# Kernel optimization log

Measured on AMD Instinct MI355X. Metric: run time of the kernel, lower is better.

Reference implementation:

```python
import jax, jax.numpy as jnp
import numpy as np

EPS = 1e-7

def _sample_project(feat, pid, w1, b1, w2, b2):
    # feat: [B, C, H, W]; pid: [P] flat spatial indices into H*W
    B, C, H, W = feat.shape
    fr = jnp.transpose(feat, (0, 2, 3, 1)).reshape(B, H * W, C)  # [B, HW, C]
    x = fr[:, pid, :].reshape(B * pid.shape[0], C)               # gather -> [B*P, C]
    x = jnp.maximum(x @ w1 + b1, 0.0) @ w2 + b2                  # 2-layer MLP
    norm = jnp.sqrt(jnp.sum(x * x, axis=1, keepdims=True))       # L2 over channels
    return x / (norm + EPS)


def setup_inputs() -> dict:
    key = jax.random.key(0)
    ks = jax.random.split(key, 16)
    NC = 256
    shapes = [(16, 256, 128, 128), (16, 512, 64, 64), (16, 1024, 32, 32)]
    inp = {}
    for i, s in enumerate(shapes):
        inp[f"feat{i}"] = jax.random.normal(ks[i], s, dtype=jnp.float32)
        hw = s[2] * s[3]
        inp[f"patch_id{i}"] = jax.random.randint(ks[3 + i], (256,), 0, hw, dtype=jnp.int64)
        C = s[1]
        g = 0.02  # init_gain (normal init)
        inp[f"w1_{i}"] = g * jax.random.normal(ks[6 + 3 * i], (C, NC), dtype=jnp.float32)
        inp[f"b1_{i}"] = jnp.zeros((NC,), dtype=jnp.float32)
        inp[f"w2_{i}"] = g * jax.random.normal(ks[7 + 3 * i], (NC, NC), dtype=jnp.float32)
        inp[f"b2_{i}"] = jnp.zeros((NC,), dtype=jnp.float32)
    return inp


def reference(feat0, feat1, feat2, patch_id0, patch_id1, patch_id2,
              w1_0, b1_0, w2_0, b2_0,
              w1_1, b1_1, w2_1, b2_1,
              w1_2, b1_2, w2_2, b2_2):
    out0 = _sample_project(feat0, patch_id0, w1_0, b1_0, w2_0, b2_0)
    out1 = _sample_project(feat1, patch_id1, w1_1, b1_1, w2_1, b2_1)
    out2 = _sample_project(feat2, patch_id2, w1_2, b1_2, w2_2, b2_2)
    return (out0, out1, out2)
```

## Files before the change

### kernel.cpp

```cpp
#include <hip/hip_runtime.h>

typedef __attribute__((ext_vector_type(8))) short short8;
typedef __attribute__((ext_vector_type(4))) float floatx4;
typedef __attribute__((ext_vector_type(4))) unsigned int uintx4;

__device__ __forceinline__ short f2bf(float f) {
    unsigned u = __builtin_bit_cast(unsigned, f);
    u = (u + 0x7FFFu + ((u >> 16) & 1u)) >> 16;
    return (short)u;
}

__global__ __launch_bounds__(256) void prep_w(
    const float* __restrict__ w10, const float* __restrict__ w11, const float* __restrict__ w12,
    const float* __restrict__ w20, const float* __restrict__ w21, const float* __restrict__ w22,
    unsigned short* __restrict__ wsb)
{
    __shared__ float tile[32][33];
    int blk = blockIdx.x;
    const float* in; unsigned short* out; int K, t0;
    if (blk < 64)       { in = w10; out = wsb;          K = 256;  t0 = 0; }
    else if (blk < 192) { in = w11; out = wsb + 65536;  K = 512;  t0 = 64; }
    else if (blk < 448) { in = w12; out = wsb + 196608; K = 1024; t0 = 192; }
    else if (blk < 512) { in = w20; out = wsb + 458752; K = 256;  t0 = 448; }
    else if (blk < 576) { in = w21; out = wsb + 524288; K = 256;  t0 = 512; }
    else                { in = w22; out = wsb + 589824; K = 256;  t0 = 576; }
    int tile_id = blk - t0;
    int tk = K >> 5;
    int k0 = (tile_id % tk) << 5;
    int n0 = (tile_id / tk) << 5;
    int t = threadIdx.x;
    int j = t & 31, i0 = (t >> 5) << 2;
    #pragma unroll
    for (int u = 0; u < 4; u++)
        tile[i0 + u][j] = in[(size_t)(k0 + i0 + u) * 256 + (n0 + j)];
    __syncthreads();
    int kf = t & 31, nf0 = (t >> 5) << 2;
    #pragma unroll
    for (int u = 0; u < 4; u++)
        out[(size_t)(n0 + nf0 + u) * K + (k0 + kf)] = (unsigned short)f2bf(tile[kf][nf0 + u]);
}

__global__ __launch_bounds__(256, 2) void fused_mlp(
    const float* __restrict__ feat0, const float* __restrict__ feat1, const float* __restrict__ feat2,
    const int* __restrict__ pid0, const int* __restrict__ pid1, const int* __restrict__ pid2,
    const float* __restrict__ b1_0, const float* __restrict__ b1_1, const float* __restrict__ b1_2,
    const float* __restrict__ b2_0, const float* __restrict__ b2_1, const float* __restrict__ b2_2,
    const unsigned short* __restrict__ wsb,
    float* __restrict__ out)
{
    __shared__ __align__(16) unsigned short smem[26944];
    unsigned short* wsS = smem;
    unsigned short* xs  = smem + 18432;
    unsigned short* hs  = smem + 18432;
    float* rs = (float*)(smem + 26880);

    int blk = blockIdx.x;
    int scale = 2 - (blk >> 7);
    int mblk = blk & 127;

    const float* feat; const int* pid; const float* b1; const float* b2;
    const unsigned short* w1T; const unsigned short* w2T;
    int C, HW; size_t outBase;
    if (scale == 0) { feat = feat0; pid = pid0; b1 = b1_0; b2 = b2_0;
                      w1T = wsb;          w2T = wsb + 458752; C = 256;  HW = 16384; outBase = 0; }
    else if (scale == 1) { feat = feat1; pid = pid1; b1 = b1_1; b2 = b2_1;
                      w1T = wsb + 65536;  w2T = wsb + 524288; C = 512;  HW = 4096;  outBase = 1048576; }
    else            { feat = feat2; pid = pid2; b1 = b1_2; b2 = b2_2;
                      w1T = wsb + 196608; w2T = wsb + 589824; C = 1024; HW = 1024;  outBase = 2097152; }

    int t = threadIdx.x;
    int wid = t >> 6, lane = t & 63, quad = lane >> 4, l15 = lane & 15;
    int r0 = (wid & 1) << 4;
    int c0 = (wid >> 1) << 7;

    int gr = t >> 3;
    int gk = (t & 7) << 3;
    int row_g = (mblk << 5) + gr;
    int bb = row_g >> 8, pp = row_g & 255;
    int s = pid[pp];
    const float* fbase = feat + (size_t)bb * ((size_t)C * HW) + s;

    floatx4 acc[8];
    #pragma unroll
    for (int f = 0; f < 8; f++) acc[f] = (floatx4){0.f, 0.f, 0.f, 0.f};

    for (int kc = 0; kc < C; kc += 64) {
        {
            const float* gp = fbase + (size_t)(kc + gk) * HW;
            float v[8];
            #pragma unroll
            for (int j2 = 0; j2 < 8; j2++) v[j2] = gp[(size_t)j2 * HW];
            short8 sv;
            #pragma unroll
            for (int j2 = 0; j2 < 8; j2++) sv[j2] = f2bf(v[j2]);
            *(short8*)(xs + gr * 72 + gk) = sv;
        }
        {
            const uintx4* src = (const uintx4*)(w1T + (size_t)t * C + kc);
            uintx4* dst = (uintx4*)(wsS + t * 72);
            #pragma unroll
            for (int j2 = 0; j2 < 8; j2++) dst[j2] = src[j2];
        }
        __syncthreads();
        const unsigned short* aRow = xs + (r0 + l15) * 72;
        const unsigned short* bRow = wsS + (c0 + l15) * 72;
        #pragma unroll
        for (int ks = 0; ks < 2; ks++) {
            short8 af = *(const short8*)(aRow + ks * 32 + quad * 8);
            #pragma unroll
            for (int f = 0; f < 8; f++) {
                short8 bf = *(const short8*)(bRow + f * (16 * 72) + ks * 32 + quad * 8);
                acc[f] = __builtin_amdgcn_mfma_f32_16x16x32_bf16(af, bf, acc[f], 0, 0, 0);
            }
        }
        __syncthreads();
    }

    {
        float bias1[8];
        #pragma unroll
        for (int f = 0; f < 8; f++) bias1[f] = b1[c0 + f * 16 + l15];
        #pragma unroll
        for (int f = 0; f < 8; f++)
            #pragma unroll
            for (int reg = 0; reg < 4; reg++) {
                float h = fmaxf(acc[f][reg] + bias1[f], 0.f);
                hs[(r0 + quad * 4 + reg) * 264 + (c0 + f * 16 + l15)] = (unsigned short)f2bf(h);
            }
    }

    #pragma unroll
    for (int f = 0; f < 8; f++) acc[f] = (floatx4){0.f, 0.f, 0.f, 0.f};
    const unsigned short* hA = hs + (r0 + l15) * 264;
    for (int kc = 0; kc < 256; kc += 64) {
        {
            const uintx4* src = (const uintx4*)(w2T + (size_t)t * 256 + kc);
            uintx4* dst = (uintx4*)(wsS + t * 72);
            #pragma unroll
            for (int j2 = 0; j2 < 8; j2++) dst[j2] = src[j2];
        }
        __syncthreads();
        const unsigned short* bRow = wsS + (c0 + l15) * 72;
        #pragma unroll
        for (int ks = 0; ks < 2; ks++) {
            short8 af = *(const short8*)(hA + kc + ks * 32 + quad * 8);
            #pragma unroll
            for (int f = 0; f < 8; f++) {
                short8 bf = *(const short8*)(bRow + f * (16 * 72) + ks * 32 + quad * 8);
                acc[f] = __builtin_amdgcn_mfma_f32_16x16x32_bf16(af, bf, acc[f], 0, 0, 0);
            }
        }
        __syncthreads();
    }

    {
        float bias2[8];
        #pragma unroll
        for (int f = 0; f < 8; f++) bias2[f] = b2[c0 + f * 16 + l15];
        float psq[4] = {0.f, 0.f, 0.f, 0.f};
        #pragma unroll
        for (int f = 0; f < 8; f++)
            #pragma unroll
            for (int reg = 0; reg < 4; reg++) {
                float yv = acc[f][reg] + bias2[f];
                acc[f][reg] = yv;
                psq[reg] += yv * yv;
            }
        #pragma unroll
        for (int m = 1; m < 16; m <<= 1)
            #pragma unroll
            for (int reg = 0; reg < 4; reg++)
                psq[reg] += __shfl_xor(psq[reg], m, 16);

        if (t < 32) rs[t] = 0.f;
        __syncthreads();
        if (l15 == 0) {
            #pragma unroll
            for (int reg = 0; reg < 4; reg++)
                atomicAdd(&rs[r0 + quad * 4 + reg], psq[reg]);
        }
        __syncthreads();

        #pragma unroll
        for (int f = 0; f < 8; f++)
            #pragma unroll
            for (int reg = 0; reg < 4; reg++) {
                int row = r0 + quad * 4 + reg;
                float inv = 1.f / (sqrtf(rs[row]) + 1e-7f);
                out[outBase + (size_t)((mblk << 5) + row) * 256 + (c0 + f * 16 + l15)] =
                    acc[f][reg] * inv;
            }
    }
}

extern "C" void kernel_launch(void* const* d_in, const int* in_sizes, int n_in,
                              void* d_out, int out_size, void* d_ws, size_t ws_size,
                              hipStream_t stream)
{
    (void)n_in; (void)out_size; (void)ws_size;
    bool dict = (in_sizes[1] == 256);
    const float *feat[3], *w1[3], *b1[3], *w2[3], *b2[3];
    const int* pid[3];
    for (int i = 0; i < 3; i++) {
        if (dict) {
            feat[i] = (const float*)d_in[i * 6 + 0];
            pid[i]  = (const int*)  d_in[i * 6 + 1];
            w1[i]   = (const float*)d_in[i * 6 + 2];
            b1[i]   = (const float*)d_in[i * 6 + 3];
            w2[i]   = (const float*)d_in[i * 6 + 4];
            b2[i]   = (const float*)d_in[i * 6 + 5];
        } else {
            feat[i] = (const float*)d_in[i];
            pid[i]  = (const int*)  d_in[3 + i];
            w1[i]   = (const float*)d_in[6 + 4 * i + 0];
            b1[i]   = (const float*)d_in[6 + 4 * i + 1];
            w2[i]   = (const float*)d_in[6 + 4 * i + 2];
            b2[i]   = (const float*)d_in[6 + 4 * i + 3];
        }
    }
    unsigned short* wsb = (unsigned short*)d_ws;
    prep_w<<<640, 256, 0, stream>>>(w1[0], w1[1], w1[2], w2[0], w2[1], w2[2], wsb);
    fused_mlp<<<384, 256, 0, stream>>>(feat[0], feat[1], feat[2],
                                       pid[0], pid[1], pid[2],
                                       b1[0], b1[1], b1[2],
                                       b2[0], b2[1], b2[2],
                                       wsb, (float*)d_out);
}
```

Baseline: 542.0 us.

## Split feature gather into separate massively parallel kernel before MLP

Measured after the change: 563.5 us. 4.0% more time.

```diff
diff --git a/kernel.cpp b/kernel.cpp
--- a/kernel.cpp
+++ b/kernel.cpp
@@ -9,6 +9,7 @@
     u = (u + 0x7FFFu + ((u >> 16) & 1u)) >> 16;
     return (short)u;
 }
+
 
 __global__ __launch_bounds__(256) void prep_w(
     const float* __restrict__ w10, const float* __restrict__ w11, const float* __restrict__ w12,
@@ -40,9 +41,36 @@
         out[(size_t)(n0 + nf0 + u) * K + (k0 + kf)] = (unsigned short)f2bf(tile[kf][nf0 + u]);
 }
 
-__global__ __launch_bounds__(256, 2) void fused_mlp(
+__global__ __launch_bounds__(256) void gather_x(
     const float* __restrict__ feat0, const float* __restrict__ feat1, const float* __restrict__ feat2,
     const int* __restrict__ pid0, const int* __restrict__ pid1, const int* __restrict__ pid2,
+    unsigned short* __restrict__ wsb)
+{
+    int blk = blockIdx.x;
+    const float* feat; const int* pid; unsigned short* xg;
+    int lblk, cl8, HW;
+    if (blk < 512)       { feat = feat0; pid = pid0; lblk = blk;        cl8 = 5; HW = 16384; xg = wsb + 655360; }
+    else if (blk < 1536) { feat = feat1; pid = pid1; lblk = blk - 512;  cl8 = 6; HW = 4096;  xg = wsb + 1703936; }
+    else                 { feat = feat2; pid = pid2; lblk = blk - 1536; cl8 = 7; HW = 1024;  xg = wsb + 3801088; }
+
+    int g   = (lblk << 8) + threadIdx.x;
+    int row = g >> cl8;
+    int gk  = (g & ((1 << cl8) - 1)) << 3;
+    int b = row >> 8, p = row & 255;
+    int s = pid[p];
+    int C = 8 << cl8;
+
+    const float* gp = feat + (size_t)b * ((size_t)C * HW) + (size_t)gk * HW + s;
+    float v[8];
+    #pragma unroll
+    for (int j = 0; j < 8; j++) v[j] = gp[(size_t)j * HW];
+    short8 sv;
+    #pragma unroll
+    for (int j = 0; j < 8; j++) sv[j] = f2bf(v[j]);
+    *(short8*)(xg + ((size_t)row << (cl8 + 3)) + gk) = sv;
+}
+
+__global__ __launch_bounds__(256, 2) void fused_mlp(
     const float* __restrict__ b1_0, const float* __restrict__ b1_1, const float* __restrict__ b1_2,
     const float* __restrict__ b2_0, const float* __restrict__ b2_1, const float* __restrict__ b2_2,
     const unsigned short* __restrict__ wsb,
@@ -58,15 +86,15 @@
     int scale = 2 - (blk >> 7);
     int mblk = blk & 127;
 
-    const float* feat; const int* pid; const float* b1; const float* b2;
-    const unsigned short* w1T; const unsigned short* w2T;
-    int C, HW; size_t outBase;
-    if (scale == 0) { feat = feat0; pid = pid0; b1 = b1_0; b2 = b2_0;
-                      w1T = wsb;          w2T = wsb + 458752; C = 256;  HW = 16384; outBase = 0; }
-    else if (scale == 1) { feat = feat1; pid = pid1; b1 = b1_1; b2 = b2_1;
-                      w1T = wsb + 65536;  w2T = wsb + 524288; C = 512;  HW = 4096;  outBase = 1048576; }
-    else            { feat = feat2; pid = pid2; b1 = b1_2; b2 = b2_2;
-                      w1T = wsb + 196608; w2T = wsb + 589824; C = 1024; HW = 1024;  outBase = 2097152; }
+    const float* b1; const float* b2;
+    const unsigned short* w1T; const unsigned short* w2T; const unsigned short* xg;
+    int C; size_t outBase;
+    if (scale == 0) { b1 = b1_0; b2 = b2_0; w1T = wsb;          w2T = wsb + 458752;
+                      xg = wsb + 655360;  C = 256;  outBase = 0; }
+    else if (scale == 1) { b1 = b1_1; b2 = b2_1; w1T = wsb + 65536;  w2T = wsb + 524288;
+                      xg = wsb + 1703936; C = 512;  outBase = 1048576; }
+    else            { b1 = b1_2; b2 = b2_2; w1T = wsb + 196608; w2T = wsb + 589824;
+                      xg = wsb + 3801088; C = 1024; outBase = 2097152; }
 
     int t = threadIdx.x;
     int wid = t >> 6, lane = t & 63, quad = lane >> 4, l15 = lane & 15;
@@ -76,25 +104,14 @@
     int gr = t >> 3;
     int gk = (t & 7) << 3;
     int row_g = (mblk << 5) + gr;
-    int bb = row_g >> 8, pp = row_g & 255;
-    int s = pid[pp];
-    const float* fbase = feat + (size_t)bb * ((size_t)C * HW) + s;
+    const unsigned short* xrow = xg + (size_t)row_g * C;
 
     floatx4 acc[8];
     #pragma unroll
     for (int f = 0; f < 8; f++) acc[f] = (floatx4){0.f, 0.f, 0.f, 0.f};
 
     for (int kc = 0; kc < C; kc += 64) {
-        {
-            const float* gp = fbase + (size_t)(kc + gk) * HW;
-            float v[8];
-            #pragma unroll
-            for (int j2 = 0; j2 < 8; j2++) v[j2] = gp[(size_t)j2 * HW];
-            short8 sv;
-            #pragma unroll
-            for (int j2 = 0; j2 < 8; j2++) sv[j2] = f2bf(v[j2]);
-            *(short8*)(xs + gr * 72 + gk) = sv;
-        }
+        *(short8*)(xs + gr * 72 + gk) = *(const short8*)(xrow + kc + gk);
         {
             const uintx4* src = (const uintx4*)(w1T + (size_t)t * C + kc);
             uintx4* dst = (uintx4*)(wsS + t * 72);
@@ -220,9 +237,9 @@
     }
     unsigned short* wsb = (unsigned short*)d_ws;
     prep_w<<<640, 256, 0, stream>>>(w1[0], w1[1], w1[2], w2[0], w2[1], w2[2], wsb);
-    fused_mlp<<<384, 256, 0, stream>>>(feat[0], feat[1], feat[2],
-                                       pid[0], pid[1], pid[2],
-                                       b1[0], b1[1], b1[2],
+    gather_x<<<3584, 256, 0, stream>>>(feat[0], feat[1], feat[2],
+                                       pid[0], pid[1], pid[2], wsb);
+    fused_mlp<<<384, 256, 0, stream>>>(b1[0], b1[1], b1[2],
                                        b2[0], b2[1], b2[2],
                                        wsb, (float*)d_out);
 }
```
